# Optimization experiments

Measured on AMD Instinct MI355X. Metric: run time of the kernel, lower is better.

The kernel has to match this reference:

```python
import jax, jax.numpy as jnp
import numpy as np

FEAT = 1433
HID = 2
NUM_CLASS = 7
EPS = 1e-5  # torch BatchNorm1d default eps


def _bn_softsign(h, gamma, beta):
    # BatchNorm1d in training mode: batch stats over (batch, length) per channel.
    mu = h.mean(axis=(0, 2), keepdims=True)
    var = h.var(axis=(0, 2), keepdims=True)  # biased, matches torch normalization
    hn = (h - mu) * jax.lax.rsqrt(var + EPS)
    hn = hn * gamma[None, :, None] + beta[None, :, None]
    return hn / (1.0 + jnp.abs(hn))  # Softsign


def feature_adjacency(x, y):
    # (x.unsqueeze(-1) * y.unsqueeze(-2)).sum(dim=1) with x channel dim == 1
    # reduces to an outer product of x[:,0] with neighbor.sum over K.
    adj = jnp.einsum('bf,bg->bfg', x.sum(1), y.sum(1))  # [B,F,F]
    adj = adj + jnp.swapaxes(adj, -1, -2)
    adj = jnp.sqrt(adj)
    # row_normalize: divide by sum over dim 1, zero out inf/nan
    norm = adj / adj.sum(axis=1, keepdims=True)
    norm = jnp.where(jnp.isfinite(norm), norm, 0.0)
    return norm + jnp.eye(FEAT, dtype=x.dtype)


def featbrd(x, adj, W, b):
    # adjacency-based feature conv: y[b,c,f] = sum_g adj[(b),f,g] x[b,c,g],
    # then 1x1 conv over channels (Conv1d kernel_size=1).
    if adj.shape[0] == 1:
        y = jnp.einsum('fg,bcg->bcf', adj[0], x)
    else:
        y = jnp.einsum('bfg,bcg->bcf', adj, x)
    return jnp.einsum('oc,bcf->bof', W, y) + b[None, :, None]


def setup_inputs() -> dict:
    key = jax.random.key(0)
    ks = jax.random.split(key, 10)
    B, K = 64, 8
    inp = {
        'x': jax.random.uniform(ks[0], (B, 1, FEAT), dtype=jnp.float32),
        'neighbor': jax.random.uniform(ks[1], (B, K, FEAT), dtype=jnp.float32),
        'adj_buf': jnp.zeros((1, FEAT, FEAT), jnp.float32),
        'W1': jax.random.normal(ks[2], (HID, 1), jnp.float32) * 0.5,
        'b1': jnp.zeros((HID,), jnp.float32),
        'W2': jax.random.normal(ks[3], (HID, HID), jnp.float32) * 0.5,
        'b2': jnp.zeros((HID,), jnp.float32),
        'g1': jnp.ones((HID,), jnp.float32),
        'be1': jnp.zeros((HID,), jnp.float32),
        'g2': jnp.ones((HID,), jnp.float32),
        'be2': jnp.zeros((HID,), jnp.float32),
        'Wc': jax.random.normal(ks[4], (NUM_CLASS, FEAT * HID), jnp.float32) * 0.02,
        'bc': jnp.zeros((NUM_CLASS,), jnp.float32),
    }
    return inp


def reference(x, neighbor, adj_buf, W1, b1, W2, b2, g1, be1, g2, be2, Wc, bc):
    fadj = feature_adjacency(x, neighbor)          # [B,F,F]
    adj_tot = adj_buf + fadj.sum(0)                # [1,F,F] (buffer starts at zero)
    h = _bn_softsign(featbrd(x, fadj, W1, b1), g1, be1)      # [B,HID,F]
    h = _bn_softsign(featbrd(h, adj_tot, W2, b2), g2, be2)   # [B,HID,F]
    flat = h.reshape(h.shape[0], -1)               # Flatten (C then F, row-major)
    return flat @ Wc.T + bc
```

## Files before the change

kernel.cpp:

```cpp
#include <hip/hip_runtime.h>
#include <hip/hip_bf16.h>
#include <math.h>

constexpr int F   = 1433;
constexpr int NB  = 64;
constexpr int KN  = 8;
constexpr int BF  = NB * F;
constexpr float EPS = 1e-5f;

constexpr int SF  = 16;
constexpr int CH  = 90;
constexpr int AbS = 1440;
constexpr int SK  = 15;
constexpr int FT  = 12;
constexpr int NA  = 720;
constexpr int NST = 256;

constexpr int O_YS  = 0;
constexpr int O_DP  = O_YS + BF;
constexpr int O_Y1P = O_DP + SF * BF;
constexpr int O_P   = O_Y1P + SF * BF;
constexpr int O_Y1  = O_P + 4 * BF;
constexpr int O_Y2  = O_Y1 + BF;
constexpr int O_G2P = O_Y2 + 2 * BF;
constexpr int O_AB  = O_G2P + SK * 128 * F;
constexpr int O_ST  = O_AB + (F * AbS) / 2;

__global__ __launch_bounds__(256) void k_ys(const float* __restrict__ nbr,
                                            float* __restrict__ ys,
                                            float* __restrict__ st) {
  if (blockIdx.x == 0 && threadIdx.x < 64) st[threadIdx.x] = 0.f;
  int i = blockIdx.x * 256 + threadIdx.x;
  if (i >= BF) return;
  int b = i / F, g = i - b * F;
  const float* p = nbr + (size_t)b * KN * F + g;
  float s = 0.f;
#pragma unroll
  for (int k = 0; k < KN; ++k) s += p[k * F];
  ys[i] = s;
}

__global__ __launch_bounds__(256) void k_D(const float* __restrict__ x,
                                           const float* __restrict__ ys,
                                           float* __restrict__ DP) {
  __shared__ __align__(8) float2 xyc[CH];
  const int b = blockIdx.x, s = blockIdx.y;
  const int cs = s * CH, cn = min(CH, F - cs);
  for (int i = threadIdx.x; i < cn; i += 256)
    xyc[i] = make_float2(x[b * F + cs + i], ys[b * F + cs + i]);
  __syncthreads();
  float gx[6], gy[6], acc[6] = {};
#pragma unroll
  for (int j = 0; j < 6; ++j) {
    int g = threadIdx.x + 256 * j;
    gx[j] = (g < F) ? x[b * F + g] : 0.f;
    gy[j] = (g < F) ? ys[b * F + g] : 0.f;
  }
#pragma unroll 6
  for (int i = 0; i < cn; ++i) {
    float2 p = xyc[i];
#pragma unroll
    for (int j = 0; j < 6; ++j)
      acc[j] += __builtin_amdgcn_sqrtf(fmaf(gy[j], p.x, gx[j] * p.y));
  }
#pragma unroll
  for (int j = 0; j < 6; ++j) {
    int g = threadIdx.x + 256 * j;
    if (g < F) DP[(size_t)s * BF + b * F + g] = acc[j];
  }
}

__global__ __launch_bounds__(256) void k_y1(const float* __restrict__ x,
                                            const float* __restrict__ ys,
                                            const float* __restrict__ DP,
                                            float* __restrict__ Y1P,
                                            float4* __restrict__ P) {
  __shared__ __align__(16) float4 pl[CH];
  const int b = blockIdx.x, s = blockIdx.y;
  const int cs = s * CH, cn = min(CH, F - cs);
  for (int i = threadIdx.x; i < cn; i += 256) {
    int g = cs + i;
    float d = 0.f;
#pragma unroll
    for (int t = 0; t < SF; ++t) d += DP[(size_t)t * BF + b * F + g];
    float inv = (d > 0.f) ? 1.f / d : 0.f;
    float xv = x[b * F + g], yv = ys[b * F + g];
    float4 pv = make_float4(xv, yv, xv * inv, inv);
    pl[i] = pv;
    P[b * F + g] = pv;
  }
  __syncthreads();
  float fx[6], fy[6], acc[6] = {};
#pragma unroll
  for (int j = 0; j < 6; ++j) {
    int f = threadIdx.x + 256 * j;
    fx[j] = (f < F) ? x[b * F + f] : 0.f;
    fy[j] = (f < F) ? ys[b * F + f] : 0.f;
  }
#pragma unroll 6
  for (int i = 0; i < cn; ++i) {
    float4 p = pl[i];
#pragma unroll
    for (int j = 0; j < 6; ++j)
      acc[j] = fmaf(__builtin_amdgcn_sqrtf(fmaf(fx[j], p.y, fy[j] * p.x)), p.z, acc[j]);
  }
#pragma unroll
  for (int j = 0; j < 6; ++j) {
    int f = threadIdx.x + 256 * j;
    if (f < F) Y1P[(size_t)s * BF + b * F + f] = acc[j];
  }
}

__global__ __launch_bounds__(256) void k_Astats(const float* __restrict__ x,
                                                const float* __restrict__ ys,
                                                const float4* __restrict__ P,
                                                const float* __restrict__ Y1P,
                                                __hip_bfloat16* __restrict__ Ab,
                                                float* __restrict__ y1,
                                                float* __restrict__ st) {
  const int bid = blockIdx.x;
  if (bid < NA) {
    __shared__ float2 fxy[FT][NB];
    const int gxc = bid % 6, fy = bid / 6;
    const int fbase = fy * FT;
#pragma unroll
    for (int r = 0; r < 3; ++r) {
      int i = threadIdx.x + 256 * r;
      int j = i >> 6, bb = i & 63;
      int f = fbase + j;
      float vx = 0.f, vy = 0.f;
      if (f < F) { vx = x[bb * F + f]; vy = ys[bb * F + f]; }
      fxy[j][bb] = make_float2(vx, vy);
    }
    __syncthreads();
    const int g = gxc * 256 + threadIdx.x;
    if (g >= AbS) return;
    if (g < F) {
      float acc[FT] = {};
      float4 pc = P[g];
#pragma unroll 2
      for (int bb = 0; bb < NB; ++bb) {
        float4 pn = pc;
        if (bb < NB - 1) pn = P[(bb + 1) * F + g];
#pragma unroll
        for (int j = 0; j < FT; ++j) {
          float2 w = fxy[j][bb];
          acc[j] = fmaf(__builtin_amdgcn_sqrtf(fmaf(w.x, pc.y, pc.x * w.y)), pc.w, acc[j]);
        }
        pc = pn;
      }
#pragma unroll
      for (int j = 0; j < FT; ++j) {
        int f = fbase + j;
        if (f < F) Ab[(size_t)f * AbS + g] = __float2bfloat16(acc[j]);
      }
    } else {
#pragma unroll
      for (int j = 0; j < FT; ++j) {
        int f = fbase + j;
        if (f < F) Ab[(size_t)f * AbS + g] = __float2bfloat16(0.f);
      }
    }
  } else {
    const int sid = bid - NA;
    float sv = 0.f, sq = 0.f;
    for (int i = sid * 256 + threadIdx.x; i < BF; i += NST * 256) {
      float v = x[i];
#pragma unroll
      for (int t = 0; t < SF; ++t) v += Y1P[(size_t)t * BF + i];
      y1[i] = v;
      sv += v; sq += v * v;
    }
#pragma unroll
    for (int o = 32; o; o >>= 1) {
      sv += __shfl_down(sv, o, 64);
      sq += __shfl_down(sq, o, 64);
    }
    __shared__ float ls[4], lq[4];
    int wave = threadIdx.x >> 6, lane = threadIdx.x & 63;
    if (lane == 0) { ls[wave] = sv; lq[wave] = sq; }
    __syncthreads();
    if (threadIdx.x == 0) {
      atomicAdd(&st[0], ls[0] + ls[1] + ls[2] + ls[3]);
      atomicAdd(&st[1], lq[0] + lq[1] + lq[2] + lq[3]);
    }
  }
}

__global__ __launch_bounds__(256) void k_gemm(const ushort* __restrict__ Ab,
                                              const float* __restrict__ y1,
                                              const float* __restrict__ st,
                                              const float* __restrict__ W1,
                                              const float* __restrict__ g1,
                                              const float* __restrict__ be1,
                                              float* __restrict__ G2P) {
  const float mu = st[0] / (float)BF;
  const float var = st[1] / (float)BF - mu * mu;
  const float wa = W1[0], wb = W1[1];
  const float k0 = wa * g1[0] / sqrtf(wa * wa * var + EPS);
  const float k1 = wb * g1[1] / sqrtf(wb * wb * var + EPS);
  const float c0 = -k0 * mu + be1[0];
  const float c1 = -k1 * mu + be1[1];

  __shared__ __align__(16) float Al[2][32 * 36];
  __shared__ __align__(16) float Hl[2][32 * 132];
  const int f0 = blockIdx.x * 32;
  const int gs = blockIdx.y * 96;
  const int tid = threadIdx.x;
  const int ffs = tid >> 3, g4s = (tid & 7) * 4;
  const int hb = tid & 7, hg = tid >> 3;
  const int fsub = (tid & 7) * 4, msub = (tid >> 3) * 4;

  uint2 pa; float pyv[8];
  auto loadRegs = [&](int gb) {
    const int f = f0 + ffs;
    pa = make_uint2(0u, 0u);
    if (f < F) pa = *(const uint2*)&Ab[(size_t)f * AbS + gb + g4s];
    const int gl = min(gb + hg, F - 1);
#pragma unroll
    for (int r = 0; r < 8; ++r) pyv[r] = y1[(hb + 8 * r) * F + gl];
  };
  auto storeLDS = [&](int buf) {
    Al[buf][(g4s + 0) * 36 + ffs] = __uint_as_float(pa.x << 16);
    Al[buf][(g4s + 1) * 36 + ffs] = __uint_as_float(pa.x & 0xffff0000u);
    Al[buf][(g4s + 2) * 36 + ffs] = __uint_as_float(pa.y << 16);
    Al[buf][(g4s + 3) * 36 + ffs] = __uint_as_float(pa.y & 0xffff0000u);
#pragma unroll
    for (int r = 0; r < 8; ++r) {
      const int bb = hb + 8 * r;
      const float v = pyv[r];
      float h0 = fmaf(k0, v, c0); h0 = h0 / (1.f + fabsf(h0));
      float h1 = fmaf(k1, v, c1); h1 = h1 / (1.f + fabsf(h1));
      *(float2*)&Hl[buf][hg * 132 + 2 * bb] = make_float2(h0, h1);
    }
  };

  float acc[4][4] = {};
  loadRegs(gs);
  storeLDS(0);
  __syncthreads();
  for (int c = 0; c < 3; ++c) {
    const int buf = c & 1;
    if (c < 2) loadRegs(gs + (c + 1) * 32);
    const float* A_ = Al[buf];
    const float* H_ = Hl[buf];
#pragma unroll 4
    for (int gi = 0; gi < 32; ++gi) {
      float4 a4 = *(const float4*)&A_[gi * 36 + fsub];
      float4 h4 = *(const float4*)&H_[gi * 132 + msub];
      float av[4] = {a4.x, a4.y, a4.z, a4.w};
      float hv[4] = {h4.x, h4.y, h4.z, h4.w};
#pragma unroll
      for (int i = 0; i < 4; ++i)
#pragma unroll
        for (int j = 0; j < 4; ++j)
          acc[i][j] = fmaf(av[i], hv[j], acc[i][j]);
    }
    if (c < 2) storeLDS(buf ^ 1);
    __syncthreads();
  }
  float* dst = G2P + (size_t)blockIdx.y * 128 * F;
#pragma unroll
  for (int i = 0; i < 4; ++i) {
    int f = f0 + fsub + i;
    if (f < F) {
#pragma unroll
      for (int j = 0; j < 4; ++j)
        dst[(msub + j) * F + f] = acc[i][j];
    }
  }
}

__global__ __launch_bounds__(256) void k_stats2(const float* __restrict__ y1,
                                                const float* __restrict__ G2P,
                                                const float* __restrict__ st,
                                                const float* __restrict__ W1,
                                                const float* __restrict__ g1,
                                                const float* __restrict__ be1,
                                                float* __restrict__ y2,
                                                float* __restrict__ stw) {
  const float mu = st[0] / (float)BF;
  const float var = st[1] / (float)BF - mu * mu;
  const float wa = W1[0], wb = W1[1];
  const float k0 = wa * g1[0] / sqrtf(wa * wa * var + EPS);
  const float k1 = wb * g1[1] / sqrtf(wb * wb * var + EPS);
  const float c0 = -k0 * mu + be1[0];
  const float c1 = -k1 * mu + be1[1];

  float su = 0.f, sv = 0.f, suu = 0.f, svv = 0.f, suv = 0.f;
  for (int i = blockIdx.x * 256 + threadIdx.x; i < BF; i += gridDim.x * 256) {
    int b = i / F, f = i - b * F;
    float w = y1[i];
    float h0 = fmaf(k0, w, c0); h0 = h0 / (1.f + fabsf(h0));
    float h1 = fmaf(k1, w, c1); h1 = h1 / (1.f + fabsf(h1));
    int iu = (2 * b) * F + f, iv = iu + F;
    float u = 64.f * h0, v = 64.f * h1;
#pragma unroll
    for (int t = 0; t < SK; ++t) {
      u += G2P[(size_t)t * 128 * F + iu];
      v += G2P[(size_t)t * 128 * F + iv];
    }
    y2[iu] = u; y2[iv] = v;
    su += u; sv += v; suu += u * u; svv += v * v; suv += u * v;
  }
#pragma unroll
  for (int o = 32; o; o >>= 1) {
    su += __shfl_down(su, o, 64);
    sv += __shfl_down(sv, o, 64);
    suu += __shfl_down(suu, o, 64);
    svv += __shfl_down(svv, o, 64);
    suv += __shfl_down(suv, o, 64);
  }
  __shared__ float red[5][4];
  int wave = threadIdx.x >> 6, lane = threadIdx.x & 63;
  if (lane == 0) {
    red[0][wave] = su; red[1][wave] = sv; red[2][wave] = suu;
    red[3][wave] = svv; red[4][wave] = suv;
  }
  __syncthreads();
  if (threadIdx.x == 0) {
#pragma unroll
    for (int m = 0; m < 5; ++m)
      atomicAdd(&stw[2 + m], red[m][0] + red[m][1] + red[m][2] + red[m][3]);
  }
}

__global__ __launch_bounds__(256) void k_out(const float* __restrict__ y2,
                                             const float* __restrict__ st,
                                             const float* __restrict__ W2,
                                             const float* __restrict__ b2,
                                             const float* __restrict__ g2,
                                             const float* __restrict__ be2,
                                             const float* __restrict__ Wc,
                                             const float* __restrict__ bc,
                                             float* __restrict__ out) {
  float n = (float)BF;
  float Eu = st[2] / n, Ev = st[3] / n;
  float Euu = st[4] / n, Evv = st[5] / n, Euv = st[6] / n;
  float cA[2], cB[2], cC[2];
#pragma unroll
  for (int o = 0; o < 2; ++o) {
    float w0 = W2[o * 2 + 0], w1 = W2[o * 2 + 1];
    float mean = w0 * Eu + w1 * Ev + b2[o];
    float Eh2 = w0 * w0 * Euu + 2.f * w0 * w1 * Euv + w1 * w1 * Evv +
                2.f * b2[o] * (w0 * Eu + w1 * Ev) + b2[o] * b2[o];
    float vr = Eh2 - mean * mean;
    float inv = g2[o] / sqrtf(vr + EPS);
    cA[o] = w0 * inv;
    cB[o] = w1 * inv;
    cC[o] = (b2[o] - mean) * inv + be2[o];
  }
  const int b = blockIdx.x;
  float acc[7] = {};
  for (int f = threadIdx.x; f < F; f += 256) {
    float u = y2[(2 * b) * F + f], v = y2[(2 * b + 1) * F + f];
    float h0 = fmaf(cA[0], u, fmaf(cB[0], v, cC[0]));
    h0 = h0 / (1.f + fabsf(h0));
    float h1 = fmaf(cA[1], u, fmaf(cB[1], v, cC[1]));
    h1 = h1 / (1.f + fabsf(h1));
#pragma unroll
    for (int o = 0; o < 7; ++o) acc[o] = fmaf(Wc[o * (2 * F) + f], h0, acc[o]);
#pragma unroll
    for (int o = 0; o < 7; ++o) acc[o] = fmaf(Wc[o * (2 * F) + F + f], h1, acc[o]);
  }
#pragma unroll
  for (int o = 0; o < 7; ++o) {
#pragma unroll
    for (int s = 32; s; s >>= 1) acc[o] += __shfl_down(acc[o], s, 64);
  }
  __shared__ float red[7][4];
  int wave = threadIdx.x >> 6, lane = threadIdx.x & 63;
  if (lane == 0) {
#pragma unroll
    for (int o = 0; o < 7; ++o) red[o][wave] = acc[o];
  }
  __syncthreads();
  if (threadIdx.x < 7) {
    int o = threadIdx.x;
    out[b * 7 + o] = red[o][0] + red[o][1] + red[o][2] + red[o][3] + bc[o];
  }
}

extern "C" void kernel_launch(void* const* d_in, const int* in_sizes, int n_in,
                              void* d_out, int out_size, void* d_ws, size_t ws_size,
                              hipStream_t stream) {
  const float* x    = (const float*)d_in[0];
  const float* nbr  = (const float*)d_in[1];
  const float* W1   = (const float*)d_in[3];
  const float* W2   = (const float*)d_in[5];
  const float* b2   = (const float*)d_in[6];
  const float* g1   = (const float*)d_in[7];
  const float* be1  = (const float*)d_in[8];
  const float* g2   = (const float*)d_in[9];
  const float* be2  = (const float*)d_in[10];
  const float* Wc   = (const float*)d_in[11];
  const float* bc   = (const float*)d_in[12];
  float* out = (float*)d_out;
  float* ws  = (float*)d_ws;

  float*  ys  = ws + O_YS;
  float*  DP  = ws + O_DP;
  float*  Y1P = ws + O_Y1P;
  float4* P   = (float4*)(ws + O_P);
  float*  y1  = ws + O_Y1;
  float*  y2  = ws + O_Y2;
  float*  G2P = ws + O_G2P;
  __hip_bfloat16* Ab = (__hip_bfloat16*)(ws + O_AB);
  float*  st  = ws + O_ST;

  k_ys    <<<(BF + 255) / 256, 256, 0, stream>>>(nbr, ys, st);
  k_D     <<<dim3(NB, SF), 256, 0, stream>>>(x, ys, DP);
  k_y1    <<<dim3(NB, SF), 256, 0, stream>>>(x, ys, DP, Y1P, P);
  k_Astats<<<NA + NST, 256, 0, stream>>>(x, ys, P, Y1P, Ab, y1, st);
  k_gemm  <<<dim3(45, SK), 256, 0, stream>>>((const ushort*)Ab, y1, st, W1, g1, be1, G2P);
  k_stats2<<<NST, 256, 0, stream>>>(y1, G2P, st, W1, g1, be1, y2, st);
  k_out   <<<NB, 256, 0, stream>>>(y2, st, W2, b2, g2, be2, Wc, bc, out);
}
```

Measured before the change: 208.2 us.

## Fuse neighbor sum into k_D, deepen prefetch in Astats, single-buffer GEMM LDS

Removes the separate k_ys launch: k_D now sums the K neighbor rows itself, recomputing them in every (b, s) block, and writes ys once from the s==0 blocks. It also zeroes the stats buffer. The A-build loop in k_Astats now prefetches four batch rows of P at a time instead of one. k_gemm drops its LDS double buffering in favour of a single buffer with an extra barrier and sets occupancy launch bounds of 4 blocks. The changes trade one saved launch and extra latency hiding against 16x redundant neighbor reads and more synchronization in the GEMM.

```diff
diff --git a/kernel.cpp b/kernel.cpp
--- a/kernel.cpp
+++ b/kernel.cpp
@@ -26,35 +26,41 @@
 constexpr int O_AB  = O_G2P + SK * 128 * F;
 constexpr int O_ST  = O_AB + (F * AbS) / 2;
 
-__global__ __launch_bounds__(256) void k_ys(const float* __restrict__ nbr,
-                                            float* __restrict__ ys,
-                                            float* __restrict__ st) {
-  if (blockIdx.x == 0 && threadIdx.x < 64) st[threadIdx.x] = 0.f;
-  int i = blockIdx.x * 256 + threadIdx.x;
-  if (i >= BF) return;
-  int b = i / F, g = i - b * F;
-  const float* p = nbr + (size_t)b * KN * F + g;
-  float s = 0.f;
-#pragma unroll
-  for (int k = 0; k < KN; ++k) s += p[k * F];
-  ys[i] = s;
-}
-
 __global__ __launch_bounds__(256) void k_D(const float* __restrict__ x,
-                                           const float* __restrict__ ys,
-                                           float* __restrict__ DP) {
+                                           const float* __restrict__ nbr,
+                                           float* __restrict__ DP,
+                                           float* __restrict__ ys_out,
+                                           float* __restrict__ st) {
+  const int b = blockIdx.x, s = blockIdx.y;
+  if (b == 0 && s == 0 && threadIdx.x < 64) st[threadIdx.x] = 0.f;
   __shared__ __align__(8) float2 xyc[CH];
-  const int b = blockIdx.x, s = blockIdx.y;
   const int cs = s * CH, cn = min(CH, F - cs);
-  for (int i = threadIdx.x; i < cn; i += 256)
-    xyc[i] = make_float2(x[b * F + cs + i], ys[b * F + cs + i]);
+  for (int i = threadIdx.x; i < cn; i += 256) {
+    const float* p = nbr + (size_t)b * KN * F + cs + i;
+    float a = 0.f;
+#pragma unroll
+    for (int k = 0; k < KN; ++k) a += p[k * F];
+    xyc[i] = make_float2(x[b * F + cs + i], a);
+  }
   __syncthreads();
   float gx[6], gy[6], acc[6] = {};
 #pragma unroll
   for (int j = 0; j < 6; ++j) {
     int g = threadIdx.x + 256 * j;
-    gx[j] = (g < F) ? x[b * F + g] : 0.f;
-    gy[j] = (g < F) ? ys[b * F + g] : 0.f;
+    int gc = min(g, F - 1);
+    const float* p = nbr + (size_t)b * KN * F + gc;
+    float a = 0.f;
+#pragma unroll
+    for (int k = 0; k < KN; ++k) a += p[k * F];
+    gx[j] = (g < F) ? x[b * F + gc] : 0.f;
+    gy[j] = (g < F) ? a : 0.f;
+  }
+  if (s == 0) {
+#pragma unroll
+    for (int j = 0; j < 6; ++j) {
+      int g = threadIdx.x + 256 * j;
+      if (g < F) ys_out[b * F + g] = gy[j];
+    }
   }
 #pragma unroll 6
   for (int i = 0; i < cn; ++i) {
@@ -137,17 +143,25 @@
     if (g >= AbS) return;
     if (g < F) {
       float acc[FT] = {};
-      float4 pc = P[g];
-#pragma unroll 2
-      for (int bb = 0; bb < NB; ++bb) {
-        float4 pn = pc;
-        if (bb < NB - 1) pn = P[(bb + 1) * F + g];
-#pragma unroll
-        for (int j = 0; j < FT; ++j) {
-          float2 w = fxy[j][bb];
-          acc[j] = fmaf(__builtin_amdgcn_sqrtf(fmaf(w.x, pc.y, pc.x * w.y)), pc.w, acc[j]);
+      float4 cur[4], nxt[4];
+#pragma unroll
+      for (int t = 0; t < 4; ++t) cur[t] = P[t * F + g];
+      for (int bb = 0; bb < NB; bb += 4) {
+        if (bb + 4 < NB) {
+#pragma unroll
+          for (int t = 0; t < 4; ++t) nxt[t] = P[(bb + 4 + t) * F + g];
         }
-        pc = pn;
+#pragma unroll
+        for (int t = 0; t < 4; ++t) {
+          float4 pc = cur[t];
+#pragma unroll
+          for (int j = 0; j < FT; ++j) {
+            float2 w = fxy[j][bb + t];
+            acc[j] = fmaf(__builtin_amdgcn_sqrtf(fmaf(w.x, pc.y, pc.x * w.y)), pc.w, acc[j]);
+          }
+        }
+#pragma unroll
+        for (int t = 0; t < 4; ++t) cur[t] = nxt[t];
       }
 #pragma unroll
       for (int j = 0; j < FT; ++j) {
@@ -187,13 +201,13 @@
   }
 }
 
-__global__ __launch_bounds__(256) void k_gemm(const ushort* __restrict__ Ab,
-                                              const float* __restrict__ y1,
-                                              const float* __restrict__ st,
-                                              const float* __restrict__ W1,
-                                              const float* __restrict__ g1,
-                                              const float* __restrict__ be1,
-                                              float* __restrict__ G2P) {
+__global__ __launch_bounds__(256, 4) void k_gemm(const ushort* __restrict__ Ab,
+                                                 const float* __restrict__ y1,
+                                                 const float* __restrict__ st,
+                                                 const float* __restrict__ W1,
+                                                 const float* __restrict__ g1,
+                                                 const float* __restrict__ be1,
+                                                 float* __restrict__ G2P) {
   const float mu = st[0] / (float)BF;
   const float var = st[1] / (float)BF - mu * mu;
   const float wa = W1[0], wb = W1[1];
@@ -202,8 +216,8 @@
   const float c0 = -k0 * mu + be1[0];
   const float c1 = -k1 * mu + be1[1];
 
-  __shared__ __align__(16) float Al[2][32 * 36];
-  __shared__ __align__(16) float Hl[2][32 * 132];
+  __shared__ __align__(16) float Al[32 * 36];
+  __shared__ __align__(16) float Hl[32 * 132];
   const int f0 = blockIdx.x * 32;
   const int gs = blockIdx.y * 96;
   const int tid = threadIdx.x;
@@ -220,34 +234,32 @@
 #pragma unroll
     for (int r = 0; r < 8; ++r) pyv[r] = y1[(hb + 8 * r) * F + gl];
   };
-  auto storeLDS = [&](int buf) {
-    Al[buf][(g4s + 0) * 36 + ffs] = __uint_as_float(pa.x << 16);
-    Al[buf][(g4s + 1) * 36 + ffs] = __uint_as_float(pa.x & 0xffff0000u);
-    Al[buf][(g4s + 2) * 36 + ffs] = __uint_as_float(pa.y << 16);
-    Al[buf][(g4s + 3) * 36 + ffs] = __uint_as_float(pa.y & 0xffff0000u);
+  auto storeLDS = [&]() {
+    Al[(g4s + 0) * 36 + ffs] = __uint_as_float(pa.x << 16);
+    Al[(g4s + 1) * 36 + ffs] = __uint_as_float(pa.x & 0xffff0000u);
+    Al[(g4s + 2) * 36 + ffs] = __uint_as_float(pa.y << 16);
+    Al[(g4s + 3) * 36 + ffs] = __uint_as_float(pa.y & 0xffff0000u);
 #pragma unroll
     for (int r = 0; r < 8; ++r) {
       const int bb = hb + 8 * r;
       const float v = pyv[r];
       float h0 = fmaf(k0, v, c0); h0 = h0 / (1.f + fabsf(h0));
       float h1 = fmaf(k1, v, c1); h1 = h1 / (1.f + fabsf(h1));
-      *(float2*)&Hl[buf][hg * 132 + 2 * bb] = make_float2(h0, h1);
+      *(float2*)&Hl[hg * 132 + 2 * bb] = make_float2(h0, h1);
     }
   };
 
   float acc[4][4] = {};
   loadRegs(gs);
-  storeLDS(0);
-  __syncthreads();
   for (int c = 0; c < 3; ++c) {
-    const int buf = c & 1;
+    if (c) __syncthreads();
+    storeLDS();
+    __syncthreads();
     if (c < 2) loadRegs(gs + (c + 1) * 32);
-    const float* A_ = Al[buf];
-    const float* H_ = Hl[buf];
 #pragma unroll 4
     for (int gi = 0; gi < 32; ++gi) {
-      float4 a4 = *(const float4*)&A_[gi * 36 + fsub];
-      float4 h4 = *(const float4*)&H_[gi * 132 + msub];
+      float4 a4 = *(const float4*)&Al[gi * 36 + fsub];
+      float4 h4 = *(const float4*)&Hl[gi * 132 + msub];
       float av[4] = {a4.x, a4.y, a4.z, a4.w};
       float hv[4] = {h4.x, h4.y, h4.z, h4.w};
 #pragma unroll
@@ -256,8 +268,6 @@
         for (int j = 0; j < 4; ++j)
           acc[i][j] = fmaf(av[i], hv[j], acc[i][j]);
     }
-    if (c < 2) storeLDS(buf ^ 1);
-    __syncthreads();
   }
   float* dst = G2P + (size_t)blockIdx.y * 128 * F;
 #pragma unroll
@@ -408,8 +418,7 @@
   __hip_bfloat16* Ab = (__hip_bfloat16*)(ws + O_AB);
   float*  st  = ws + O_ST;
 
-  k_ys    <<<(BF + 255) / 256, 256, 0, stream>>>(nbr, ys, st);
-  k_D     <<<dim3(NB, SF), 256, 0, stream>>>(x, ys, DP);
+  k_D     <<<dim3(NB, SF), 256, 0, stream>>>(x, nbr, DP, ys, st);
   k_y1    <<<dim3(NB, SF), 256, 0, stream>>>(x, ys, DP, Y1P, P);
   k_Astats<<<NA + NST, 256, 0, stream>>>(x, ys, P, Y1P, Ab, y1, st);
   k_gemm  <<<dim3(45, SK), 256, 0, stream>>>((const ushort*)Ab, y1, st, W1, g1, be1, G2P);
```

New measurement: 204.8 us, median of 2. No clear change (-1.6%).
